# Kernel tuning notes

Measured on AMD Instinct MI355X. Metric: run time of the kernel, lower is better.

The kernel has to match this reference:

```python
import jax, jax.numpy as jnp
import numpy as np

B = 8192
D = 256
T_PRIME_INIT = 2.302585  # log(10)
B_INIT = -10.0


def setup_inputs() -> dict:
    key = jax.random.key(0)
    k1, k2 = jax.random.split(key)
    return {
        "loc_month_emb": jax.random.normal(k1, (B, D), dtype=jnp.float32),
        "chelsa_emb": jax.random.normal(k2, (B, D), dtype=jnp.float32),
        "t_prime": jnp.full((1,), T_PRIME_INIT, dtype=jnp.float32),
        "b": jnp.full((1,), B_INIT, dtype=jnp.float32),
    }


def reference(loc_month_emb, chelsa_emb, t_prime, b):
    batchsize = loc_month_emb.shape[0]
    # L2-normalize each embedding row
    loc = loc_month_emb / jnp.linalg.norm(loc_month_emb, axis=-1, keepdims=True)
    che = chelsa_emb / jnp.linalg.norm(chelsa_emb, axis=-1, keepdims=True)
    # [B, B] pairwise logits, scaled by exp(t') and shifted by b
    logits = jnp.einsum("id,jd->ij", che, loc) * jnp.exp(t_prime) + b
    # labels: +1 on diagonal, -1 off-diagonal
    labels = jnp.eye(batchsize, dtype=logits.dtype) * 2.0 - 1.0
    # log(1/(1+exp(-y*z))) == log_sigmoid(y*z)
    loss_matrix = jax.nn.log_sigmoid(labels * logits)
    loss = -jnp.sum(loss_matrix) / batchsize
    return loss
```

## Files before the change

kernel.cpp:

```cpp
#include <hip/hip_runtime.h>
#include <hip/hip_bf16.h>

typedef __attribute__((ext_vector_type(4))) int   i32x4;
typedef __attribute__((ext_vector_type(4))) float f32x4;

#define BATCH 8192
#define DIM   256

#define QMAX   0.4f
#define QSTEP  (QMAX / 127.0f)

__global__ __launch_bounds__(256) void normalize_kernel(
    const float* __restrict__ che, const float* __restrict__ loc,
    char* __restrict__ qA, char* __restrict__ qB,
    float* __restrict__ out)
{
    if (blockIdx.x == 0 && threadIdx.x == 0) out[0] = 0.f;

    int wave = threadIdx.x >> 6;
    int lane = threadIdx.x & 63;
    int base = (blockIdx.x * 4 + wave) * 4;

    const float* src; char* dst; int row;
    if (base < BATCH) { src = che; dst = qA; row = base; }
    else              { src = loc; dst = qB; row = base - BATCH; }

    float4 v[4];
#pragma unroll
    for (int j = 0; j < 4; j++)
        v[j] = ((const float4*)(src + (size_t)(row + j) * DIM))[lane];

    float ss[4];
#pragma unroll
    for (int j = 0; j < 4; j++)
        ss[j] = v[j].x*v[j].x + v[j].y*v[j].y + v[j].z*v[j].z + v[j].w*v[j].w;
#pragma unroll
    for (int off = 1; off < 64; off <<= 1) {
#pragma unroll
        for (int j = 0; j < 4; j++) ss[j] += __shfl_xor(ss[j], off, 64);
    }

#pragma unroll
    for (int j = 0; j < 4; j++) {
        float qs = rsqrtf(ss[j]) * (127.0f / QMAX);
        float f0 = fminf(127.f, fmaxf(-127.f, rintf(v[j].x * qs)));
        float f1 = fminf(127.f, fmaxf(-127.f, rintf(v[j].y * qs)));
        float f2 = fminf(127.f, fmaxf(-127.f, rintf(v[j].z * qs)));
        float f3 = fminf(127.f, fmaxf(-127.f, rintf(v[j].w * qs)));
        int q0 = (int)f0, q1 = (int)f1, q2 = (int)f2, q3 = (int)f3;
        int packed = (q0 & 255) | ((q1 & 255) << 8) | ((q2 & 255) << 16) | (q3 << 24);
        ((int*)(dst + (size_t)(row + j) * DIM))[lane] = packed;
    }
}

__device__ __forceinline__ void gload_lds16(const void* g, void* l) {
    __builtin_amdgcn_global_load_lds(
        (const __attribute__((address_space(1))) void*)g,
        (__attribute__((address_space(3))) void*)l, 16, 0, 0);
}

__global__ __launch_bounds__(512) void gemm_loss_kernel(
    const char* __restrict__ Aq,
    const char* __restrict__ Bq,
    const float* __restrict__ tp, const float* __restrict__ bb,
    float* __restrict__ out)
{
    __shared__ __align__(16) char ldsA[65536];
    __shared__ __align__(16) char ldsB[65536];
    __shared__ float red[8];

    const int tid  = threadIdx.x;
    const int wave = tid >> 6;
    const int lane = tid & 63;
    const int wm = wave >> 2, wn = wave & 3;
    const int r15 = lane & 15;
    const int q16 = (lane >> 4) << 4;
    const int swz = (lane & 7) << 4;

    const int trow     = blockIdx.x >> 3;
    const int tcolBase = (blockIdx.x & 7) << 2;
    const int brow     = trow << 8;

    {
        const int rowA = tid >> 4;
        const int kbA  = ((tid & 15) << 4) ^ ((rowA & 7) << 4);
        const char* src = Aq + (size_t)(brow + rowA) * 256 + kbA;
        char* dst = ldsA + tid * 16;
#pragma unroll
        for (int p = 0; p < 8; p++)
            gload_lds16(src + p * 8192, dst + p * 8192);
    }

    const int rowB = tid >> 3;
    const int kbB  = ((tid & 7) << 4) ^ ((rowB & 7) << 4);
    const char* pBsrc = Bq + (size_t)rowB * 256 + kbB;
    char* pBdstT = ldsB + tid * 16;

#define STAGE_B(G) do {                                                       \
        int _ti = (G) >> 1, _s = (G) & 1;                                     \
        const char* _src = pBsrc + (size_t)((tcolBase + _ti) << 8) * 256      \
                         + _s * 128;                                          \
        char* _dst = pBdstT + ((G) & 1) * 32768;                              \
        _Pragma("unroll")                                                     \
        for (int _p = 0; _p < 4; _p++)                                        \
            gload_lds16(_src + _p * 16384, _dst + _p * 8192);                 \
    } while (0)

    STAGE_B(0);

    const char* aBase = ldsA + (size_t)(wm * 128 + r15) * 256;
    int bRow[4];
#pragma unroll
    for (int n = 0; n < 4; n++) bRow[n] = (wn * 64 + n * 16 + r15) * 128;

    const float scale = __expf(tp[0]);
    const float shift = bb[0];
    const float LOG2E = 1.44269504f;
    const float S2 = QSTEP * QSTEP;
    const float W  = S2 * scale * LOG2E;
    const float K0 = shift * LOG2E;
    const float DZ = S2 * scale;
    const int lr = (lane >> 4) * 4;

    float local = 0.f;

    i32x4 acc[8][4];
#pragma unroll
    for (int m = 0; m < 8; m++)
#pragma unroll
        for (int n = 0; n < 4; n++) acc[m][n] = (i32x4){0, 0, 0, 0};

#pragma unroll
    for (int ti = 0; ti < 4; ti++) {
#pragma unroll
        for (int s = 0; s < 2; s++) {
            const int g = ti * 2 + s;
            asm volatile("s_waitcnt vmcnt(0)" ::: "memory");
            __builtin_amdgcn_s_barrier();
            __builtin_amdgcn_sched_barrier(0);
            if (g < 7) STAGE_B(g + 1);
            __builtin_amdgcn_sched_barrier(0);

            const char* bufB = ldsB + (g & 1) * 32768;
#pragma unroll
            for (int ks = 0; ks < 2; ks++) {
                const int koA = (s * 128 + ks * 64 + q16) ^ swz;
                const int koB = (ks * 64 + q16) ^ swz;
                i32x4 a[8], b[4];
#pragma unroll
                for (int n = 0; n < 4; n++)
                    b[n] = *(const i32x4*)(bufB + bRow[n] + koB);
#pragma unroll
                for (int m = 0; m < 8; m++)
                    a[m] = *(const i32x4*)(aBase + m * 4096 + koA);
#pragma unroll
                for (int m = 0; m < 8; m++)
#pragma unroll
                    for (int n = 0; n < 4; n++)
                        acc[m][n] = __builtin_amdgcn_mfma_i32_16x16x64_i8(
                            a[m], b[n], acc[m][n], 0, 0, 0);
            }
        }

        const bool diagTile = (trow == tcolBase + ti);
#pragma unroll
        for (int m = 0; m < 8; m++) {
#pragma unroll
            for (int n = 0; n < 4; n++) {
                const bool fdiag = diagTile && (wm * 128 + m * 16 == wn * 64 + n * 16);
#pragma unroll
                for (int r = 0; r < 4; r++) {
                    float ci = (float)acc[m][n][r];
                    local += __builtin_amdgcn_exp2f(fmaf(ci, W, K0));
                    if (fdiag && r15 == lr + r)
                        local -= fmaf(ci, DZ, shift);
                    acc[m][n][r] = 0;
                }
            }
        }
    }

#pragma unroll
    for (int off = 32; off; off >>= 1) local += __shfl_down(local, off, 64);
    if (lane == 0) red[wave] = local;
    __syncthreads();
    if (tid == 0) {
        float s = 0.f;
#pragma unroll
        for (int w = 0; w < 8; w++) s += red[w];
        atomicAdd(out, s * (1.0f / (float)BATCH));
    }
#undef STAGE_B
}

extern "C" void kernel_launch(void* const* d_in, const int* in_sizes, int n_in,
                              void* d_out, int out_size, void* d_ws, size_t ws_size,
                              hipStream_t stream) {
    const float* loc = (const float*)d_in[0];
    const float* che = (const float*)d_in[1];
    const float* tp  = (const float*)d_in[2];
    const float* bb  = (const float*)d_in[3];
    float* out = (float*)d_out;

    char* qA = (char*)d_ws;
    char* qB = qA + (size_t)BATCH * DIM;

    normalize_kernel<<<1024, 256, 0, stream>>>(che, loc, qA, qB, out);
    gemm_loss_kernel<<<256, 512, 0, stream>>>(qA, qB, tp, bb, out);
}
```

Measured before the change: 96.11 us.

## Stream A and B k-slices through 64KB LDS and double block count

Instead of keeping the full 256x256 A tile resident in LDS and streaming B, each block now streams 64-wide K slices of both A and B through a shared double-buffered 64KB LDS region with a new XOR swizzle. Each block covers two column tiles instead of four, so the grid grows from 256 to 512 blocks, and launch bounds request more occupancy. The aim is to cut LDS use so more blocks fit per CU and to spread the work over more CUs. In exchange, A is reloaded from global/L2 for every column tile, and there are more barriers.

Result: slower. 194.1 us (+101.9%).

```diff
diff --git a/kernel.cpp b/kernel.cpp
--- a/kernel.cpp
+++ b/kernel.cpp
@@ -59,15 +59,13 @@
         (__attribute__((address_space(3))) void*)l, 16, 0, 0);
 }
 
-__global__ __launch_bounds__(512) void gemm_loss_kernel(
+__global__ __launch_bounds__(512, 4) void gemm_loss_kernel(
     const char* __restrict__ Aq,
     const char* __restrict__ Bq,
     const float* __restrict__ tp, const float* __restrict__ bb,
     float* __restrict__ out)
 {
-    __shared__ __align__(16) char ldsA[65536];
-    __shared__ __align__(16) char ldsB[65536];
-    __shared__ float red[8];
+    __shared__ __align__(16) char lds[65536];
 
     const int tid  = threadIdx.x;
     const int wave = tid >> 6;
@@ -75,43 +73,28 @@
     const int wm = wave >> 2, wn = wave & 3;
     const int r15 = lane & 15;
     const int q16 = (lane >> 4) << 4;
-    const int swz = (lane & 7) << 4;
+    const int swz = (((r15 & 3) ^ ((r15 >> 2) & 1)) << 4);
 
-    const int trow     = blockIdx.x >> 3;
-    const int tcolBase = (blockIdx.x & 7) << 2;
-    const int brow     = trow << 8;
+    const int trow  = blockIdx.x >> 4;
+    const int cg    = blockIdx.x & 15;
+    const int brow  = trow << 8;
 
-    {
-        const int rowA = tid >> 4;
-        const int kbA  = ((tid & 15) << 4) ^ ((rowA & 7) << 4);
-        const char* src = Aq + (size_t)(brow + rowA) * 256 + kbA;
-        char* dst = ldsA + tid * 16;
-#pragma unroll
-        for (int p = 0; p < 8; p++)
-            gload_lds16(src + p * 8192, dst + p * 8192);
-    }
+    const int srow  = tid >> 2;
+    const int skb   = (((tid & 3) ^ ((tid >> 2) & 3) ^ ((tid >> 4) & 1)) << 4);
+    const char* pAsrc = Aq + (size_t)(brow + srow) * 256 + skb;
+    const char* pBsrc = Bq + (size_t)srow * 256 + skb;
+    char* dstT = lds + tid * 16;
 
-    const int rowB = tid >> 3;
-    const int kbB  = ((tid & 7) << 4) ^ ((rowB & 7) << 4);
-    const char* pBsrc = Bq + (size_t)rowB * 256 + kbB;
-    char* pBdstT = ldsB + tid * 16;
-
-#define STAGE_B(G) do {                                                       \
-        int _ti = (G) >> 1, _s = (G) & 1;                                     \
-        const char* _src = pBsrc + (size_t)((tcolBase + _ti) << 8) * 256      \
-                         + _s * 128;                                          \
-        char* _dst = pBdstT + ((G) & 1) * 32768;                              \
-        _Pragma("unroll")                                                     \
-        for (int _p = 0; _p < 4; _p++)                                        \
-            gload_lds16(_src + _p * 16384, _dst + _p * 8192);                 \
+#define STAGE(G) do {                                                         \
+        const int _tl = (G) >> 2, _k = ((G) & 3) * 64;                        \
+        const size_t _bc = (size_t)((2 * cg + _tl) << 8) * 256;               \
+        char* _dA = dstT + ((G) & 1) * 16384;                                 \
+        char* _dB = _dA + 32768;                                              \
+        gload_lds16(pAsrc + _k, _dA);                                         \
+        gload_lds16(pAsrc + 128 * 256 + _k, _dA + 8192);                      \
+        gload_lds16(pBsrc + _bc + _k, _dB);                                   \
+        gload_lds16(pBsrc + _bc + 128 * 256 + _k, _dB + 8192);                \
     } while (0)
-
-    STAGE_B(0);
-
-    const char* aBase = ldsA + (size_t)(wm * 128 + r15) * 256;
-    int bRow[4];
-#pragma unroll
-    for (int n = 0; n < 4; n++) bRow[n] = (wn * 64 + n * 16 + r15) * 128;
 
     const float scale = __expf(tp[0]);
     const float shift = bb[0];
@@ -130,51 +113,53 @@
 #pragma unroll
         for (int n = 0; n < 4; n++) acc[m][n] = (i32x4){0, 0, 0, 0};
 
+    STAGE(0);
+
+    const int aRow0 = (wm * 128 + r15) * 64;
+    const int bRow0 = (wn * 64 + r15) * 64;
+    const int ko = q16 ^ swz;
+
 #pragma unroll
-    for (int ti = 0; ti < 4; ti++) {
+    for (int g = 0; g < 8; ++g) {
+        asm volatile("s_waitcnt vmcnt(0)" ::: "memory");
+        __builtin_amdgcn_s_barrier();
+        __builtin_amdgcn_sched_barrier(0);
+        if (g < 7) STAGE(g + 1);
+        __builtin_amdgcn_sched_barrier(0);
+
+        const char* bufA = lds + (g & 1) * 16384;
+        const char* bufB = bufA + 32768;
+        i32x4 a[8], b[4];
 #pragma unroll
-        for (int s = 0; s < 2; s++) {
-            const int g = ti * 2 + s;
-            asm volatile("s_waitcnt vmcnt(0)" ::: "memory");
-            __builtin_amdgcn_s_barrier();
-            __builtin_amdgcn_sched_barrier(0);
-            if (g < 7) STAGE_B(g + 1);
-            __builtin_amdgcn_sched_barrier(0);
+        for (int n = 0; n < 4; n++)
+            b[n] = *(const i32x4*)(bufB + bRow0 + n * 1024 + ko);
+#pragma unroll
+        for (int m = 0; m < 8; m++)
+            a[m] = *(const i32x4*)(bufA + aRow0 + m * 1024 + ko);
+#pragma unroll
+        for (int m = 0; m < 8; m++)
+#pragma unroll
+            for (int n = 0; n < 4; n++)
+                acc[m][n] = __builtin_amdgcn_mfma_i32_16x16x64_i8(
+                    a[m], b[n], acc[m][n], 0, 0, 0);
 
-            const char* bufB = ldsB + (g & 1) * 32768;
+        if ((g & 3) == 3) {
+            const int tl = g >> 2;
+            const bool diagTile = (trow == 2 * cg + tl);
 #pragma unroll
-            for (int ks = 0; ks < 2; ks++) {
-                const int koA = (s * 128 + ks * 64 + q16) ^ swz;
-                const int koB = (ks * 64 + q16) ^ swz;
-                i32x4 a[8], b[4];
+            for (int m = 0; m < 8; m++) {
 #pragma unroll
-                for (int n = 0; n < 4; n++)
-                    b[n] = *(const i32x4*)(bufB + bRow[n] + koB);
+                for (int n = 0; n < 4; n++) {
+                    const bool fdiag = diagTile &&
+                        (wm * 128 + m * 16 == wn * 64 + n * 16);
 #pragma unroll
-                for (int m = 0; m < 8; m++)
-                    a[m] = *(const i32x4*)(aBase + m * 4096 + koA);
-#pragma unroll
-                for (int m = 0; m < 8; m++)
-#pragma unroll
-                    for (int n = 0; n < 4; n++)
-                        acc[m][n] = __builtin_amdgcn_mfma_i32_16x16x64_i8(
-                            a[m], b[n], acc[m][n], 0, 0, 0);
-            }
-        }
-
-        const bool diagTile = (trow == tcolBase + ti);
-#pragma unroll
-        for (int m = 0; m < 8; m++) {
-#pragma unroll
-            for (int n = 0; n < 4; n++) {
-                const bool fdiag = diagTile && (wm * 128 + m * 16 == wn * 64 + n * 16);
-#pragma unroll
-                for (int r = 0; r < 4; r++) {
-                    float ci = (float)acc[m][n][r];
-                    local += __builtin_amdgcn_exp2f(fmaf(ci, W, K0));
-                    if (fdiag && r15 == lr + r)
-                        local -= fmaf(ci, DZ, shift);
-                    acc[m][n][r] = 0;
+                    for (int r = 0; r < 4; r++) {
+                        float ci = (float)acc[m][n][r];
+                        local += __builtin_amdgcn_exp2f(fmaf(ci, W, K0));
+                        if (fdiag && r15 == lr + r)
+                            local -= fmaf(ci, DZ, shift);
+                        acc[m][n][r] = 0;
+                    }
                 }
             }
         }
@@ -182,6 +167,8 @@
 
 #pragma unroll
     for (int off = 32; off; off >>= 1) local += __shfl_down(local, off, 64);
+    __syncthreads();
+    float* red = (float*)lds;
     if (lane == 0) red[wave] = local;
     __syncthreads();
     if (tid == 0) {
@@ -190,7 +177,7 @@
         for (int w = 0; w < 8; w++) s += red[w];
         atomicAdd(out, s * (1.0f / (float)BATCH));
     }
-#undef STAGE_B
+#undef STAGE
 }
 
 extern "C" void kernel_launch(void* const* d_in, const int* in_sizes, int n_in,
@@ -206,5 +193,5 @@
     char* qB = qA + (size_t)BATCH * DIM;
 
     normalize_kernel<<<1024, 256, 0, stream>>>(che, loc, qA, qB, out);
-    gemm_loss_kernel<<<256, 512, 0, stream>>>(qA, qB, tp, bb, out);
+    gemm_loss_kernel<<<512, 512, 0, stream>>>(qA, qB, tp, bb, out);
 }
```
